# Kernel tuning notes

Measured on AMD Instinct MI355X. Metric: run time of the kernel, lower is better.

Reference implementation:

```python
import jax, jax.numpy as jnp
import numpy as np

INPUT_DIM = 512
DEGREE = 3
NUM_KNOTS = 16
NUM_NEURONS = 1024
OUTPUT_DIM = 512
NUM_BASIS = NUM_KNOTS + DEGREE - 1  # 18


def make_knots():
    # uniform grid on [0,1], extended by `degree` knots on each side
    h = 1.0 / (NUM_KNOTS - 1)
    grid = np.linspace(0.0, 1.0, NUM_KNOTS)
    lo = grid[0] - h * np.arange(DEGREE, 0, -1)
    hi = grid[-1] + h * np.arange(1, DEGREE + 1)
    return jnp.asarray(np.concatenate([lo, grid, hi]), dtype=jnp.float32)  # [NUM_KNOTS+2*DEGREE]


def bspline_basis(x, t, degree):
    # x: [B, N]; t: [K] uniform extended knots. Cox-de Boor recursion.
    K = t.shape[0]
    xb = x[..., None]
    B = ((xb >= t[:-1]) & (xb < t[1:])).astype(x.dtype)  # [B, N, K-1]
    for p in range(1, degree + 1):
        ti = t[: K - p - 1]
        tip = t[p : K - 1]
        ti1 = t[1 : K - p]
        tip1 = t[p + 1 : K]
        left = (xb - ti) / (tip - ti) * B[..., :-1]
        right = (tip1 - xb) / (tip1 - ti1) * B[..., 1:]
        B = left + right
    return B  # [B, N, K-1-degree] == [B, N, NUM_BASIS]


def norm_layer(x, eps=1e-8):
    # per-row min-max normalization into the spline domain [0,1)
    mn = jnp.min(x, axis=-1, keepdims=True)
    mx = jnp.max(x, axis=-1, keepdims=True)
    return (x - mn) / (mx - mn + eps)


def setup_inputs() -> dict:
    key = jax.random.key(0)
    ks = jax.random.split(key, 7)
    x = jax.random.normal(ks[0], (4096, INPUT_DIM), dtype=jnp.float32)
    s1 = 1.0 / np.sqrt(INPUT_DIM)
    s2 = 1.0 / np.sqrt(NUM_NEURONS)
    W1 = jax.random.uniform(ks[1], (INPUT_DIM, NUM_NEURONS), jnp.float32, -s1, s1)
    b1 = jax.random.uniform(ks[2], (NUM_NEURONS,), jnp.float32, -s1, s1)
    coeff = jax.random.normal(ks[3], (NUM_NEURONS, NUM_BASIS), dtype=jnp.float32) * 0.1
    sp_bias = jnp.zeros((NUM_NEURONS,), dtype=jnp.float32)
    W2 = jax.random.uniform(ks[4], (NUM_NEURONS, OUTPUT_DIM), jnp.float32, -s2, s2)
    b2 = jax.random.uniform(ks[5], (OUTPUT_DIM,), jnp.float32, -s2, s2)
    return {"x": x, "W1": W1, "b1": b1, "coeff": coeff, "sp_bias": sp_bias, "W2": W2, "b2": b2}


def reference(x, W1, b1, coeff, sp_bias, W2, b2):
    t = make_knots()
    h = x @ W1 + b1                      # [B, N]  Linear 1
    h = norm_layer(h)                    # NormLayer -> [0,1)
    basis = bspline_basis(h, t, DEGREE)  # [B, N, NUM_BASIS]
    sp = jnp.einsum('bnk,nk->bn', basis, coeff) + sp_bias  # per-neuron spline eval
    out = sp @ W2 + b2                   # Linear 2
    return jax.nn.relu(out)
```

## Files before the change

### kernel.cpp

```cpp
#include <hip/hip_runtime.h>

#define M_ROWS  4096
#define IN_DIM  512
#define NEURONS 1024
#define OUT_DIM 512

typedef _Float16 f16;
typedef __attribute__((ext_vector_type(8))) _Float16 f16x8;
typedef __attribute__((ext_vector_type(4))) _Float16 f16x4;
typedef __attribute__((ext_vector_type(4))) float    f32x4;

__global__ __launch_bounds__(256) void prep(
    const float* __restrict__ x,  f16* __restrict__ xh,
    const float* __restrict__ W1, f16* __restrict__ W1t,
    const float* __restrict__ W2, f16* __restrict__ W2t)
{
    __shared__ float S[32][33];
    const int b = blockIdx.x, t = threadIdx.x;
    if (b < 1024) {
        int i = b * 256 + t;
        const float4* p = (const float4*)x;
        float4 a = p[i * 2], c = p[i * 2 + 1];
        f16x8 o = { (f16)a.x, (f16)a.y, (f16)a.z, (f16)a.w,
                    (f16)c.x, (f16)c.y, (f16)c.z, (f16)c.w };
        *(f16x8*)(xh + (size_t)i * 8) = o;
        return;
    }
    const float* src; f16* dst; int R, C, tile;
    if (b < 1536) { src = W1; dst = W1t; R = IN_DIM;  C = NEURONS; tile = b - 1024; }
    else          { src = W2; dst = W2t; R = NEURONS; C = OUT_DIM; tile = b - 1536; }
    const int ntx = C / 32;
    const int tx = tile % ntx, ty = tile / ntx;
    const int tr = t >> 3, tc = (t & 7) * 4;
    float4 v = *(const float4*)&src[(size_t)(ty * 32 + tr) * C + tx * 32 + tc];
    S[tr][tc + 0] = v.x; S[tr][tc + 1] = v.y;
    S[tr][tc + 2] = v.z; S[tr][tc + 3] = v.w;
    __syncthreads();
    f16x4 o = { (f16)S[tc + 0][tr], (f16)S[tc + 1][tr],
                (f16)S[tc + 2][tr], (f16)S[tc + 3][tr] };
    *(f16x4*)&dst[(size_t)(tx * 32 + tr) * R + ty * 32 + tc] = o;
}

template<int BM, int BN, int MI, int NJ, bool RELU>
__global__ __launch_bounds__(256) void gemm_f16(
    const f16* __restrict__ A, const f16* __restrict__ Bt,
    const float* __restrict__ bias, float* __restrict__ C,
    int M, int N, int K)
{
    constexpr int nA = BM / 64;
    constexpr int nB = BN / 64;
    __shared__ f16 lds[2][(BM + BN) * 32];

    const int t    = threadIdx.x;
    const int lane = t & 63;
    const int l15  = lane & 15;
    const int lhi  = lane >> 4;
    const int wid  = t >> 6;
    const int wm   = wid >> 1, wn = wid & 1;

    const int nwg  = gridDim.x * gridDim.y;
    const int flat = blockIdx.y * gridDim.x + blockIdx.x;
    const int swz  = (flat & 7) * (nwg >> 3) + (flat >> 3);
    const int m0   = (swz / gridDim.x) * BM;
    const int n0   = (swz % gridDim.x) * BN;

    const int srow = lane >> 2;
    const int skb  = (lane & 3) * 8;

    auto stage = [&](int buf, int kt) {
        f16* base = &lds[buf][0];
#pragma unroll
        for (int j = 0; j < nA; ++j) {
            int chunk = wid * nA + j;
            const f16* g = A + (size_t)(m0 + chunk * 16 + srow) * K + kt + skb;
            __builtin_amdgcn_global_load_lds(
                (const __attribute__((address_space(1))) void*)g,
                (__attribute__((address_space(3))) void*)(base + chunk * 512),
                16, 0, 0);
        }
#pragma unroll
        for (int j = 0; j < nB; ++j) {
            int chunk = wid * nB + j;
            const f16* g = Bt + (size_t)(n0 + chunk * 16 + srow) * K + kt + skb;
            __builtin_amdgcn_global_load_lds(
                (const __attribute__((address_space(1))) void*)g,
                (__attribute__((address_space(3))) void*)(base + BM * 32 + chunk * 512),
                16, 0, 0);
        }
    };

    f32x4 acc[MI][NJ];
#pragma unroll
    for (int i = 0; i < MI; ++i)
#pragma unroll
        for (int j = 0; j < NJ; ++j) acc[i][j] = (f32x4)0.f;

    const int T = K / 32;
    stage(0, 0);
    __syncthreads();

    int cur = 0;
    for (int tt = 0; tt < T; ++tt) {
        if (tt + 1 < T) stage(cur ^ 1, (tt + 1) * 32);
        const f16* L = &lds[cur][0];
        f16x8 bfr[NJ];
#pragma unroll
        for (int nj = 0; nj < NJ; ++nj)
            bfr[nj] = *(const f16x8*)
                &L[BM * 32 + (wn * NJ * 16 + nj * 16 + l15) * 32 + lhi * 8];
#pragma unroll
        for (int mi = 0; mi < MI; ++mi) {
            f16x8 afr = *(const f16x8*)
                &L[(wm * MI * 16 + mi * 16 + l15) * 32 + lhi * 8];
#pragma unroll
            for (int nj = 0; nj < NJ; ++nj)
                acc[mi][nj] = __builtin_amdgcn_mfma_f32_16x16x32_f16(
                    afr, bfr[nj], acc[mi][nj], 0, 0, 0);
        }
        __syncthreads();
        cur ^= 1;
    }

#pragma unroll
    for (int mi = 0; mi < MI; ++mi) {
#pragma unroll
        for (int nj = 0; nj < NJ; ++nj) {
            int row0 = m0 + wm * MI * 16 + mi * 16 + lhi * 4;
            int col  = n0 + wn * NJ * 16 + nj * 16 + l15;
            float bv = bias[col];
#pragma unroll
            for (int j = 0; j < 4; ++j) {
                float v = acc[mi][nj][j] + bv;
                if (RELU) v = fmaxf(v, 0.f);
                C[(size_t)(row0 + j) * N + col] = v;
            }
        }
    }
}

__global__ __launch_bounds__(256) void norm_spline(
    const float* __restrict__ H, const float* __restrict__ coeff,
    const float* __restrict__ spb, f16* __restrict__ SPH)
{
    const int row = blockIdx.x;
    const int tid = threadIdx.x;
    const float* hr = H + (size_t)row * NEURONS;

    float4 v = reinterpret_cast<const float4*>(hr)[tid];
    float lmn = fminf(fminf(v.x, v.y), fminf(v.z, v.w));
    float lmx = fmaxf(fmaxf(v.x, v.y), fmaxf(v.z, v.w));
#pragma unroll
    for (int m = 32; m; m >>= 1) {
        lmn = fminf(lmn, __shfl_xor(lmn, m));
        lmx = fmaxf(lmx, __shfl_xor(lmx, m));
    }
    __shared__ float smn[4], smx[4];
    if ((tid & 63) == 0) { smn[tid >> 6] = lmn; smx[tid >> 6] = lmx; }
    __syncthreads();
    const float mn = fminf(fminf(smn[0], smn[1]), fminf(smn[2], smn[3]));
    const float mx = fmaxf(fmaxf(smx[0], smx[1]), fmaxf(smx[2], smx[3]));
    const float inv = 1.0f / (mx - mn + 1e-8f);

    const float hk = 1.0f / 15.0f;
    const float vv[4] = {v.x, v.y, v.z, v.w};
    float out[4];

#pragma unroll
    for (int e = 0; e < 4; ++e) {
        const int n = tid * 4 + e;
        const float u = (vv[e] - mn) * inv;
        int ii = (int)floorf(u * 15.0f);
        ii = ii < 0 ? 0 : (ii > 14 ? 14 : ii);
        const int i = ii + 3;

        float Bv[4] = {1.f, 0.f, 0.f, 0.f};
#pragma unroll
        for (int p = 1; p <= 3; ++p) {
            const float dinv = 1.0f / ((float)p * hk);
            float nb[4];
#pragma unroll
            for (int j = 3; j >= 0; --j) {
                if (j > p) { nb[j] = 0.f; continue; }
                const int m = i - p + j;
                const float tm   = (float)(m - 3) * hk;
                const float tmp1 = (float)(m + p + 1 - 3) * hk;
                const float left  = (j > 0) ? (u - tm)   * Bv[j - 1] : 0.f;
                const float right = (j < p) ? (tmp1 - u) * Bv[j]     : 0.f;
                nb[j] = (left + right) * dinv;
            }
#pragma unroll
            for (int j = 0; j < 4; ++j) Bv[j] = nb[j];
        }

        const float* c = coeff + (size_t)n * 18 + ii;
        out[e] = fmaf(Bv[0], c[0],
                 fmaf(Bv[1], c[1],
                 fmaf(Bv[2], c[2], Bv[3] * c[3]))) + spb[n];
    }
    f16x4 o = { (f16)out[0], (f16)out[1], (f16)out[2], (f16)out[3] };
    ((f16x4*)(SPH + (size_t)row * NEURONS))[tid] = o;
}

extern "C" void kernel_launch(void* const* d_in, const int* in_sizes, int n_in,
                              void* d_out, int out_size, void* d_ws, size_t ws_size,
                              hipStream_t stream)
{
    const float* x     = (const float*)d_in[0];
    const float* W1    = (const float*)d_in[1];
    const float* b1    = (const float*)d_in[2];
    const float* coeff = (const float*)d_in[3];
    const float* spb   = (const float*)d_in[4];
    const float* W2    = (const float*)d_in[5];
    const float* b2    = (const float*)d_in[6];
    float* out = (float*)d_out;

    char* ws = (char*)d_ws;
    float* h   = (float*)ws;
    f16*   xh  = (f16*)(ws + (16u << 20));
    f16*   W1t = (f16*)(ws + (20u << 20));
    f16*   W2t = (f16*)(ws + (22u << 20));
    f16*   sph = (f16*)(ws + (23u << 20));

    prep<<<dim3(2048), 256, 0, stream>>>(x, xh, W1, W1t, W2, W2t);

    gemm_f16<128, 64, 4, 2, false><<<dim3(NEURONS / 64, M_ROWS / 128), 256, 0, stream>>>(
        xh, W1t, b1, h, M_ROWS, NEURONS, IN_DIM);

    norm_spline<<<dim3(M_ROWS), 256, 0, stream>>>(h, coeff, spb, sph);

    gemm_f16<64, 64, 2, 2, true><<<dim3(OUT_DIM / 64, M_ROWS / 64), 256, 0, stream>>>(
        sph, W2t, b2, out, M_ROWS, OUT_DIM, NEURONS);
}
```

Baseline: 54.35 us.

## Fuse row min/max into GEMM1 epilogue, store H as fp16, widen K tile

GEMM1 now writes the hidden activations as fp16 and computes per-row min/max in its epilogue via shuffle reduction plus atomicMin/atomicMax on order-preserving integer keys, which prep initializes. norm_spline then reads only the precomputed extrema and the half-size H, and drops its block reduction and barrier. Both GEMMs move from a K-step of 32 to 64 per LDS stage, halving the number of barriers. The risks are extra atomic traffic, fp16 rounding of H before normalization, and the larger LDS footprint per block.

Result: no change. 53.48 us (-1.6%).

```diff
diff --git a/kernel.cpp b/kernel.cpp
--- a/kernel.cpp
+++ b/kernel.cpp
@@ -10,10 +10,20 @@
 typedef __attribute__((ext_vector_type(4))) _Float16 f16x4;
 typedef __attribute__((ext_vector_type(4))) float    f32x4;
 
+__device__ __forceinline__ unsigned fkey(float f) {
+    unsigned b = __float_as_uint(f);
+    return b ^ ((b & 0x80000000u) ? 0xFFFFFFFFu : 0x80000000u);
+}
+__device__ __forceinline__ float fdec(unsigned k) {
+    unsigned b = (k & 0x80000000u) ? (k ^ 0x80000000u) : ~k;
+    return __uint_as_float(b);
+}
+
 __global__ __launch_bounds__(256) void prep(
     const float* __restrict__ x,  f16* __restrict__ xh,
     const float* __restrict__ W1, f16* __restrict__ W1t,
-    const float* __restrict__ W2, f16* __restrict__ W2t)
+    const float* __restrict__ W2, f16* __restrict__ W2t,
+    unsigned* __restrict__ keys)
 {
     __shared__ float S[32][33];
     const int b = blockIdx.x, t = threadIdx.x;
@@ -24,6 +34,11 @@
         f16x8 o = { (f16)a.x, (f16)a.y, (f16)a.z, (f16)a.w,
                     (f16)c.x, (f16)c.y, (f16)c.z, (f16)c.w };
         *(f16x8*)(xh + (size_t)i * 8) = o;
+        return;
+    }
+    if (b >= 2048) {
+        int i = (b - 2048) * 256 + t;
+        keys[i] = (i < 4096) ? 0xFFFFFFFFu : 0u;
         return;
     }
     const float* src; f16* dst; int R, C, tile;
@@ -41,15 +56,16 @@
     *(f16x4*)&dst[(size_t)(tx * 32 + tr) * R + ty * 32 + tc] = o;
 }
 
-template<int BM, int BN, int MI, int NJ, bool RELU>
-__global__ __launch_bounds__(256) void gemm_f16(
+template<int BM, int BN, int MI, int NJ, int OUTMODE>
+__global__ __launch_bounds__(256) void gemm_f16k64(
     const f16* __restrict__ A, const f16* __restrict__ Bt,
-    const float* __restrict__ bias, float* __restrict__ C,
+    const float* __restrict__ bias, void* __restrict__ Cout,
+    unsigned* __restrict__ minkey, unsigned* __restrict__ maxkey,
     int M, int N, int K)
 {
-    constexpr int nA = BM / 64;
-    constexpr int nB = BN / 64;
-    __shared__ f16 lds[2][(BM + BN) * 32];
+    constexpr int CA = BM / 32;
+    constexpr int CB = BN / 32;
+    __shared__ f16 lds[2][(BM + BN) * 64];
 
     const int t    = threadIdx.x;
     const int lane = t & 63;
@@ -64,27 +80,24 @@
     const int m0   = (swz / gridDim.x) * BM;
     const int n0   = (swz % gridDim.x) * BN;
 
-    const int srow = lane >> 2;
-    const int skb  = (lane & 3) * 8;
-
     auto stage = [&](int buf, int kt) {
         f16* base = &lds[buf][0];
 #pragma unroll
-        for (int j = 0; j < nA; ++j) {
-            int chunk = wid * nA + j;
-            const f16* g = A + (size_t)(m0 + chunk * 16 + srow) * K + kt + skb;
+        for (int j = 0; j < CA; ++j) {
+            int c = wid * CA + j;
+            const f16* g = A + (size_t)(m0 + c * 8 + (lane >> 3)) * K + kt + (lane & 7) * 8;
             __builtin_amdgcn_global_load_lds(
                 (const __attribute__((address_space(1))) void*)g,
-                (__attribute__((address_space(3))) void*)(base + chunk * 512),
+                (__attribute__((address_space(3))) void*)(base + c * 512),
                 16, 0, 0);
         }
 #pragma unroll
-        for (int j = 0; j < nB; ++j) {
-            int chunk = wid * nB + j;
-            const f16* g = Bt + (size_t)(n0 + chunk * 16 + srow) * K + kt + skb;
+        for (int j = 0; j < CB; ++j) {
+            int c = wid * CB + j;
+            const f16* g = Bt + (size_t)(n0 + c * 8 + (lane >> 3)) * K + kt + (lane & 7) * 8;
             __builtin_amdgcn_global_load_lds(
                 (const __attribute__((address_space(1))) void*)g,
-                (__attribute__((address_space(3))) void*)(base + BM * 32 + chunk * 512),
+                (__attribute__((address_space(3))) void*)(base + BM * 64 + c * 512),
                 16, 0, 0);
         }
     };
@@ -95,27 +108,30 @@
 #pragma unroll
         for (int j = 0; j < NJ; ++j) acc[i][j] = (f32x4)0.f;
 
-    const int T = K / 32;
+    const int T = K / 64;
     stage(0, 0);
     __syncthreads();
 
     int cur = 0;
     for (int tt = 0; tt < T; ++tt) {
-        if (tt + 1 < T) stage(cur ^ 1, (tt + 1) * 32);
+        if (tt + 1 < T) stage(cur ^ 1, (tt + 1) * 64);
         const f16* L = &lds[cur][0];
-        f16x8 bfr[NJ];
-#pragma unroll
-        for (int nj = 0; nj < NJ; ++nj)
-            bfr[nj] = *(const f16x8*)
-                &L[BM * 32 + (wn * NJ * 16 + nj * 16 + l15) * 32 + lhi * 8];
-#pragma unroll
-        for (int mi = 0; mi < MI; ++mi) {
-            f16x8 afr = *(const f16x8*)
-                &L[(wm * MI * 16 + mi * 16 + l15) * 32 + lhi * 8];
+#pragma unroll
+        for (int ks = 0; ks < 2; ++ks) {
+            f16x8 bfr[NJ];
 #pragma unroll
             for (int nj = 0; nj < NJ; ++nj)
-                acc[mi][nj] = __builtin_amdgcn_mfma_f32_16x16x32_f16(
-                    afr, bfr[nj], acc[mi][nj], 0, 0, 0);
+                bfr[nj] = *(const f16x8*)
+                    &L[BM * 64 + (wn * NJ * 16 + nj * 16 + l15) * 64 + ks * 32 + lhi * 8];
+#pragma unroll
+            for (int mi = 0; mi < MI; ++mi) {
+                f16x8 afr = *(const f16x8*)
+                    &L[(wm * MI * 16 + mi * 16 + l15) * 64 + ks * 32 + lhi * 8];
+#pragma unroll
+                for (int nj = 0; nj < NJ; ++nj)
+                    acc[mi][nj] = __builtin_amdgcn_mfma_f32_16x16x32_f16(
+                        afr, bfr[nj], acc[mi][nj], 0, 0, 0);
+            }
         }
         __syncthreads();
         cur ^= 1;
@@ -123,52 +139,73 @@
 
 #pragma unroll
     for (int mi = 0; mi < MI; ++mi) {
-#pragma unroll
-        for (int nj = 0; nj < NJ; ++nj) {
-            int row0 = m0 + wm * MI * 16 + mi * 16 + lhi * 4;
-            int col  = n0 + wn * NJ * 16 + nj * 16 + l15;
-            float bv = bias[col];
+        const int row0 = m0 + wm * MI * 16 + mi * 16 + lhi * 4;
+        if (OUTMODE == 0) {
+            f16* H = (f16*)Cout;
+            float vmn[4], vmx[4];
+#pragma unroll
+            for (int nj = 0; nj < NJ; ++nj) {
+                int col = n0 + wn * NJ * 16 + nj * 16 + l15;
+                float bv = bias[col];
+#pragma unroll
+                for (int j = 0; j < 4; ++j) {
+                    f16 hv = (f16)(acc[mi][nj][j] + bv);
+                    H[(size_t)(row0 + j) * N + col] = hv;
+                    float vr = (float)hv;
+                    if (nj == 0) { vmn[j] = vr; vmx[j] = vr; }
+                    else { vmn[j] = fminf(vmn[j], vr); vmx[j] = fmaxf(vmx[j], vr); }
+                }
+            }
 #pragma unroll
             for (int j = 0; j < 4; ++j) {
-                float v = acc[mi][nj][j] + bv;
-                if (RELU) v = fmaxf(v, 0.f);
-                C[(size_t)(row0 + j) * N + col] = v;
+#pragma unroll
+                for (int d = 1; d < 16; d <<= 1) {
+                    vmn[j] = fminf(vmn[j], __shfl_xor(vmn[j], d));
+                    vmx[j] = fmaxf(vmx[j], __shfl_xor(vmx[j], d));
+                }
+            }
+            if (l15 == 0) {
+#pragma unroll
+                for (int j = 0; j < 4; ++j) {
+                    atomicMin(&minkey[row0 + j], fkey(vmn[j]));
+                    atomicMax(&maxkey[row0 + j], fkey(vmx[j]));
+                }
+            }
+        } else {
+            float* O = (float*)Cout;
+#pragma unroll
+            for (int nj = 0; nj < NJ; ++nj) {
+                int col = n0 + wn * NJ * 16 + nj * 16 + l15;
+                float bv = bias[col];
+#pragma unroll
+                for (int j = 0; j < 4; ++j) {
+                    float v = fmaxf(acc[mi][nj][j] + bv, 0.f);
+                    O[(size_t)(row0 + j) * N + col] = v;
+                }
             }
         }
     }
 }
 
 __global__ __launch_bounds__(256) void norm_spline(
-    const float* __restrict__ H, const float* __restrict__ coeff,
+    const f16* __restrict__ H, const unsigned* __restrict__ minkey,
+    const unsigned* __restrict__ maxkey, const float* __restrict__ coeff,
     const float* __restrict__ spb, f16* __restrict__ SPH)
 {
-    const int row = blockIdx.x;
-    const int tid = threadIdx.x;
-    const float* hr = H + (size_t)row * NEURONS;
-
-    float4 v = reinterpret_cast<const float4*>(hr)[tid];
-    float lmn = fminf(fminf(v.x, v.y), fminf(v.z, v.w));
-    float lmx = fmaxf(fmaxf(v.x, v.y), fmaxf(v.z, v.w));
-#pragma unroll
-    for (int m = 32; m; m >>= 1) {
-        lmn = fminf(lmn, __shfl_xor(lmn, m));
-        lmx = fmaxf(lmx, __shfl_xor(lmx, m));
-    }
-    __shared__ float smn[4], smx[4];
-    if ((tid & 63) == 0) { smn[tid >> 6] = lmn; smx[tid >> 6] = lmx; }
-    __syncthreads();
-    const float mn = fminf(fminf(smn[0], smn[1]), fminf(smn[2], smn[3]));
-    const float mx = fmaxf(fmaxf(smx[0], smx[1]), fmaxf(smx[2], smx[3]));
+    const int row = blockIdx.x * 2 + (threadIdx.x >> 7);
+    const int t   = threadIdx.x & 127;
+    const float mn = fdec(minkey[row]);
+    const float mx = fdec(maxkey[row]);
     const float inv = 1.0f / (mx - mn + 1e-8f);
 
+    f16x8 hv = *(const f16x8*)&H[(size_t)row * NEURONS + t * 8];
     const float hk = 1.0f / 15.0f;
-    const float vv[4] = {v.x, v.y, v.z, v.w};
-    float out[4];
-
-#pragma unroll
-    for (int e = 0; e < 4; ++e) {
-        const int n = tid * 4 + e;
-        const float u = (vv[e] - mn) * inv;
+    f16x8 o;
+
+#pragma unroll
+    for (int e = 0; e < 8; ++e) {
+        const int n = t * 8 + e;
+        const float u = ((float)hv[e] - mn) * inv;
         int ii = (int)floorf(u * 15.0f);
         ii = ii < 0 ? 0 : (ii > 14 ? 14 : ii);
         const int i = ii + 3;
@@ -193,12 +230,12 @@
         }
 
         const float* c = coeff + (size_t)n * 18 + ii;
-        out[e] = fmaf(Bv[0], c[0],
-                 fmaf(Bv[1], c[1],
-                 fmaf(Bv[2], c[2], Bv[3] * c[3]))) + spb[n];
-    }
-    f16x4 o = { (f16)out[0], (f16)out[1], (f16)out[2], (f16)out[3] };
-    ((f16x4*)(SPH + (size_t)row * NEURONS))[tid] = o;
+        float sp = fmaf(Bv[0], c[0],
+                   fmaf(Bv[1], c[1],
+                   fmaf(Bv[2], c[2], Bv[3] * c[3]))) + spb[n];
+        o[e] = (f16)sp;
+    }
+    *(f16x8*)&SPH[(size_t)row * NEURONS + t * 8] = o;
 }
 
 extern "C" void kernel_launch(void* const* d_in, const int* in_sizes, int n_in,
@@ -215,19 +252,22 @@
     float* out = (float*)d_out;
 
     char* ws = (char*)d_ws;
-    float* h   = (float*)ws;
-    f16*   xh  = (f16*)(ws + (16u << 20));
-    f16*   W1t = (f16*)(ws + (20u << 20));
-    f16*   W2t = (f16*)(ws + (22u << 20));
-    f16*   sph = (f16*)(ws + (23u << 20));
-
-    prep<<<dim3(2048), 256, 0, stream>>>(x, xh, W1, W1t, W2, W2t);
-
-    gemm_f16<128, 64, 4, 2, false><<<dim3(NEURONS / 64, M_ROWS / 128), 256, 0, stream>>>(
-        xh, W1t, b1, h, M_ROWS, NEURONS, IN_DIM);
-
-    norm_spline<<<dim3(M_ROWS), 256, 0, stream>>>(h, coeff, spb, sph);
-
-    gemm_f16<64, 64, 2, 2, true><<<dim3(OUT_DIM / 64, M_ROWS / 64), 256, 0, stream>>>(
-        sph, W2t, b2, out, M_ROWS, OUT_DIM, NEURONS);
-}
+    f16*      h    = (f16*)ws;
+    f16*      sph  = (f16*)(ws + (8u  << 20));
+    f16*      xh   = (f16*)(ws + (16u << 20));
+    f16*      W1t  = (f16*)(ws + (20u << 20));
+    f16*      W2t  = (f16*)(ws + (21u << 20));
+    unsigned* keys = (unsigned*)(ws + (22u << 20));
+    unsigned* minkey = keys;
+    unsigned* maxkey = keys + 4096;
+
+    prep<<<dim3(2080), 256, 0, stream>>>(x, xh, W1, W1t, W2, W2t, keys);
+
+    gemm_f16k64<128, 64, 4, 2, 0><<<dim3(NEURONS / 64, M_ROWS / 128), 256, 0, stream>>>(
+        xh, W1t, b1, h, minkey, maxkey, M_ROWS, NEURONS, IN_DIM);
+
+    norm_spline<<<dim3(M_ROWS / 2), 256, 0, stream>>>(h, minkey, maxkey, coeff, spb, sph);
+
+    gemm_f16k64<64, 64, 2, 2, 1><<<dim3(OUT_DIM / 64, M_ROWS / 64), 256, 0, stream>>>(
+        sph, W2t, b2, out, nullptr, nullptr, M_ROWS, OUT_DIM, NEURONS);
+}
```
